# Kernel optimization log

Measured on AMD Instinct MI355X. Metric: run time of the kernel, lower is better.

Reference implementation:

```python
import jax, jax.numpy as jnp
import numpy as np

B, C, N = 32, 128, 64
HID = 2 * C
STEEPNESS = 50.0


def _bitonic_layers(n):
    """Index pairs (a, b) for each compare-exchange layer of a bitonic sorting
    network, matching diffsort's bitonic_network construction."""
    num_blocks = int(np.log2(n))
    assert n == 2 ** num_blocks
    layers = []
    for block in range(num_blocks):
        for layer in range(block + 1):
            m = 2 ** (block - layer)
            a_idx, b_idx = [], []
            for i in range(0, n, 2 * m):
                for j in range(m):
                    ix = i + j
                    a, b = ix, ix + m
                    # alternate direction within bitonic blocks
                    if (ix // 2 ** (block + 1)) % 2 == 1:
                        a, b = b, a
                    a_idx.append(a)
                    b_idx.append(b)
            layers.append((np.asarray(a_idx), np.asarray(b_idx)))
    return layers

_LAYERS = _bitonic_layers(N)  # 21 layers for N=64


def _diff_sort(scores):
    """Differentiable bitonic sort (diffsort, distribution='cauchy').
    Returns (soft-sorted scores, soft permutation matrix P) with
    sorted = scores @ P; the module applies P via bmm(P, rows)."""
    b, n = scores.shape
    x = scores
    P = jnp.broadcast_to(jnp.eye(n, dtype=scores.dtype), (b, n, n))
    inv_pi = 1.0 / np.pi
    for a_idx, b_idx in _LAYERS:
        xa, xb = x[:, a_idx], x[:, b_idx]
        alpha = jnp.arctan((xb - xa) * STEEPNESS) * inv_pi + 0.5  # Cauchy CDF
        x = x.at[:, a_idx].set(alpha * xa + (1.0 - alpha) * xb)
        x = x.at[:, b_idx].set((1.0 - alpha) * xa + alpha * xb)
        Pa, Pb = P[:, :, a_idx], P[:, :, b_idx]
        al = alpha[:, None, :]
        P = P.at[:, :, a_idx].set(al * Pa + (1.0 - al) * Pb)
        P = P.at[:, :, b_idx].set((1.0 - al) * Pa + al * Pb)
    return x, P


def setup_inputs() -> dict:
    key = jax.random.key(0)
    ks = jax.random.split(key, 9)
    s = 0.05  # keep score magnitudes reasonable under steepness=50
    return {
        "x": jax.random.normal(ks[0], (B, C, N, N), jnp.float32),
        "w1": jax.random.normal(ks[1], (HID, C), jnp.float32) * s,
        "b1": jax.random.normal(ks[2], (HID,), jnp.float32) * s,
        "w2": jax.random.normal(ks[3], (HID, HID), jnp.float32) * s,
        "b2": jax.random.normal(ks[4], (HID,), jnp.float32) * s,
        "w_row": jax.random.normal(ks[5], (HID, N), jnp.float32) * s,
        "b_row": jax.random.normal(ks[6], (1,), jnp.float32) * s,
        "w_col": jax.random.normal(ks[7], (HID, N), jnp.float32) * s,
        "b_col": jax.random.normal(ks[8], (1,), jnp.float32) * s,
    }


def reference(x, w1, b1, w2, b2, w_row, b_row, w_col, b_col):
    # feat_extractor: two 1x1 convs (pointwise channel GEMMs) + ReLU
    h = jax.nn.relu(jnp.einsum('bchw,oc->bohw', x, w1) + b1[None, :, None, None])
    h = jax.nn.relu(jnp.einsum('bchw,oc->bohw', h, w2) + b2[None, :, None, None])

    # row branch: Conv1d(HID*N,1,1) over flattened (channel, width) per row
    row_scores = jnp.einsum('bchw,cw->bh', h, w_row) + b_row  # (B, N)
    _, p_row = _diff_sort(row_scores)
    x = jnp.einsum('bij,bcjk->bcik', p_row, x)  # bmm(P_row, x) per channel

    # col branch: Conv1d(HID*N,1,1) over flattened (channel, height) per column
    col_scores = jnp.einsum('bchw,ch->bw', h, w_col) + b_col  # (B, N)
    _, p_col = _diff_sort(col_scores)
    # original: bmm(P_col, x^T) then view as (B,C,N,N) with NO transpose back
    x = jnp.einsum('bij,bckj->bcik', p_col, x)
    return x
```

## Files before the change

kernel.cpp:

```cpp
#include <hip/hip_runtime.h>
#include <math.h>

#define B_    32
#define C_    128
#define N_    64
#define HID_  256
#define PIX_  4096
#define STEEP 50.0f
#define INV_PI 0.318309886183790671f
#define LDH   272
#define LDX   72

typedef unsigned short u16;
typedef __attribute__((ext_vector_type(8))) short bf16x8;
typedef __attribute__((ext_vector_type(4))) float f32x4;

__device__ __forceinline__ u16 f2bf(float f) {
    unsigned int u = __builtin_bit_cast(unsigned int, f);
    unsigned int r = (u + 0x7FFFu + ((u >> 16) & 1u)) >> 16;
    return (u16)r;
}
__device__ __forceinline__ float bf2f(u16 h) {
    unsigned int u = ((unsigned int)h) << 16;
    return __builtin_bit_cast(float, u);
}
__device__ __forceinline__ int h1_idx(int p, int k) {
    return p * LDH + (((k >> 3) + (p & 7)) & 31) * 8 + (k & 7);
}
__device__ __forceinline__ int x_idx(int p, int k) {
    return p * LDH + 128 + (((k >> 3) + (p & 7)) & 15) * 8 + (k & 7);
}

__global__ void k_prep(const float* __restrict__ w1, const float* __restrict__ w2,
                       u16* __restrict__ w1h, u16* __restrict__ w1l,
                       u16* __restrict__ w2h, u16* __restrict__ w2l,
                       float* __restrict__ col_s, const float* __restrict__ b_col) {
    int i = blockIdx.x * 256 + threadIdx.x;
    if (i < B_ * N_) col_s[i] = b_col[0];
    if (i < HID_ * C_) {
        float v = w1[i];
        u16 h = f2bf(v);
        w1h[i] = h;
        w1l[i] = f2bf(v - bf2f(h));
    } else {
        int j = i - HID_ * C_;
        if (j < HID_ * HID_) {
            float v = w2[j];
            u16 h = f2bf(v);
            w2h[j] = h;
            w2l[j] = f2bf(v - bf2f(h));
        }
    }
}

__global__ __launch_bounds__(512) void k12_fused(
    const float* __restrict__ x,
    const u16* __restrict__ w1h, const u16* __restrict__ w1l,
    const float* __restrict__ b1,
    const u16* __restrict__ w2h, const u16* __restrict__ w2l,
    const float* __restrict__ b2, const float* __restrict__ w_row,
    const float* __restrict__ b_row, const float* __restrict__ w_col,
    float* __restrict__ row_s, float* __restrict__ col_s) {
    __shared__ __align__(16) u16 Lh[64 * LDH];
    __shared__ __align__(16) u16 Ll[64 * LDH];
    __shared__ float col_red[64];
    __shared__ float row_red;

    const int t = threadIdx.x;
    const int l = t & 63, w = t >> 6;
    const int col = l & 15, q = l >> 4;
    const int hrow = blockIdx.x;
    const int b = blockIdx.y;
    const float* xb = x + (size_t)b * C_ * PIX_ + hrow * 64;

    if (t < 64) col_red[t] = 0.f;
    if (t == 0) row_red = 0.f;

    {
        const int pt = t & 15, ct = t >> 4;
#pragma unroll
        for (int cc = 0; cc < 2; cc++) {
            const int c = cc * 64 + 2 * ct;
            float4 v0 = *(const float4*)&xb[(size_t)c * PIX_ + pt * 4];
            float4 v1 = *(const float4*)&xb[(size_t)(c + 1) * PIX_ + pt * 4];
            float a0[4] = {v0.x, v0.y, v0.z, v0.w};
            float a1[4] = {v1.x, v1.y, v1.z, v1.w};
#pragma unroll
            for (int j = 0; j < 4; j++) {
                int p = pt * 4 + j;
                u16 h0 = f2bf(a0[j]), h1v = f2bf(a1[j]);
                u16 l0 = f2bf(a0[j] - bf2f(h0)), l1 = f2bf(a1[j] - bf2f(h1v));
                int idx = x_idx(p, c);
                *(unsigned int*)&Lh[idx] = (unsigned int)h0 | ((unsigned int)h1v << 16);
                *(unsigned int*)&Ll[idx] = (unsigned int)l0 | ((unsigned int)l1 << 16);
            }
        }
    }
    __syncthreads();

    f32x4 acc[2][4];
#pragma unroll
    for (int i = 0; i < 2; i++)
#pragma unroll
        for (int j = 0; j < 4; j++) acc[i][j] = (f32x4){0.f, 0.f, 0.f, 0.f};

    bf16x8 ah[2], al_[2];
#pragma unroll
    for (int mf = 0; mf < 2; mf++) {
        size_t ro = (size_t)(32 * w + 16 * mf + col) * C_ + q * 8;
        ah[mf] = *(const bf16x8*)&w1h[ro];
        al_[mf] = *(const bf16x8*)&w1l[ro];
    }
#pragma unroll
    for (int kc = 0; kc < 4; kc++) {
        bf16x8 bh[4], bl[4];
#pragma unroll
        for (int nt = 0; nt < 4; nt++) {
            int idx = x_idx(nt * 16 + col, kc * 32 + q * 8);
            bh[nt] = *(const bf16x8*)&Lh[idx];
            bl[nt] = *(const bf16x8*)&Ll[idx];
        }
        bf16x8 ahn[2], aln[2];
        const int kn = (kc + 1) & 3;
#pragma unroll
        for (int mf = 0; mf < 2; mf++) {
            size_t ro = (size_t)(32 * w + 16 * mf + col) * C_ + kn * 32 + q * 8;
            ahn[mf] = *(const bf16x8*)&w1h[ro];
            aln[mf] = *(const bf16x8*)&w1l[ro];
        }
#pragma unroll
        for (int mf = 0; mf < 2; mf++)
#pragma unroll
            for (int nt = 0; nt < 4; nt++) {
                acc[mf][nt] = __builtin_amdgcn_mfma_f32_16x16x32_bf16(ah[mf], bh[nt], acc[mf][nt], 0, 0, 0);
                acc[mf][nt] = __builtin_amdgcn_mfma_f32_16x16x32_bf16(ah[mf], bl[nt], acc[mf][nt], 0, 0, 0);
                acc[mf][nt] = __builtin_amdgcn_mfma_f32_16x16x32_bf16(al_[mf], bh[nt], acc[mf][nt], 0, 0, 0);
            }
#pragma unroll
        for (int mf = 0; mf < 2; mf++) { ah[mf] = ahn[mf]; al_[mf] = aln[mf]; }
    }

    bf16x8 ah2[2], al2[2];
#pragma unroll
    for (int mf = 0; mf < 2; mf++) {
        size_t ro = (size_t)(32 * w + 16 * mf + col) * HID_ + q * 8;
        ah2[mf] = *(const bf16x8*)&w2h[ro];
        al2[mf] = *(const bf16x8*)&w2l[ro];
    }
    __syncthreads();

#pragma unroll
    for (int mf = 0; mf < 2; mf++) {
        int o = 32 * w + 16 * mf + q * 4;
        float bias[4];
#pragma unroll
        for (int r = 0; r < 4; r++) bias[r] = b1[o + r];
#pragma unroll
        for (int nt = 0; nt < 4; nt++) {
            int p = nt * 16 + col;
            u16 hh[4], ll[4];
#pragma unroll
            for (int r = 0; r < 4; r++) {
                float v = fmaxf(acc[mf][nt][r] + bias[r], 0.f);
                u16 h = f2bf(v);
                hh[r] = h;
                ll[r] = f2bf(v - bf2f(h));
            }
            int idx = h1_idx(p, o);
            *(unsigned long long*)&Lh[idx] =
                (unsigned long long)hh[0] | ((unsigned long long)hh[1] << 16) |
                ((unsigned long long)hh[2] << 32) | ((unsigned long long)hh[3] << 48);
            *(unsigned long long*)&Ll[idx] =
                (unsigned long long)ll[0] | ((unsigned long long)ll[1] << 16) |
                ((unsigned long long)ll[2] << 32) | ((unsigned long long)ll[3] << 48);
        }
    }
    __syncthreads();

    f32x4 acc2[2][4];
#pragma unroll
    for (int i = 0; i < 2; i++)
#pragma unroll
        for (int j = 0; j < 4; j++) acc2[i][j] = (f32x4){0.f, 0.f, 0.f, 0.f};

#pragma unroll
    for (int kc = 0; kc < 8; kc++) {
        bf16x8 bh[4], bl[4];
#pragma unroll
        for (int nt = 0; nt < 4; nt++) {
            int idx = h1_idx(nt * 16 + col, kc * 32 + q * 8);
            bh[nt] = *(const bf16x8*)&Lh[idx];
            bl[nt] = *(const bf16x8*)&Ll[idx];
        }
        bf16x8 ahn[2], aln[2];
        const int kn = (kc + 1) & 7;
#pragma unroll
        for (int mf = 0; mf < 2; mf++) {
            size_t ro = (size_t)(32 * w + 16 * mf + col) * HID_ + kn * 32 + q * 8;
            ahn[mf] = *(const bf16x8*)&w2h[ro];
            aln[mf] = *(const bf16x8*)&w2l[ro];
        }
#pragma unroll
        for (int mf = 0; mf < 2; mf++)
#pragma unroll
            for (int nt = 0; nt < 4; nt++) {
                acc2[mf][nt] = __builtin_amdgcn_mfma_f32_16x16x32_bf16(ah2[mf], bh[nt], acc2[mf][nt], 0, 0, 0);
                acc2[mf][nt] = __builtin_amdgcn_mfma_f32_16x16x32_bf16(ah2[mf], bl[nt], acc2[mf][nt], 0, 0, 0);
                acc2[mf][nt] = __builtin_amdgcn_mfma_f32_16x16x32_bf16(al2[mf], bh[nt], acc2[mf][nt], 0, 0, 0);
            }
#pragma unroll
        for (int mf = 0; mf < 2; mf++) { ah2[mf] = ahn[mf]; al2[mf] = aln[mf]; }
    }

    float rpart = 0.f;
    float cpart[4] = {0.f, 0.f, 0.f, 0.f};
#pragma unroll
    for (int mf = 0; mf < 2; mf++) {
        int o = 32 * w + 16 * mf + q * 4;
#pragma unroll
        for (int r = 0; r < 4; r++) {
            float bias = b2[o + r];
            float wcv = w_col[(o + r) * N_ + hrow];
#pragma unroll
            for (int nt = 0; nt < 4; nt++) {
                int wc = nt * 16 + col;
                float v = fmaxf(acc2[mf][nt][r] + bias, 0.f);
                rpart += v * w_row[(o + r) * N_ + wc];
                cpart[nt] += v * wcv;
            }
        }
    }
#pragma unroll
    for (int off = 32; off; off >>= 1) rpart += __shfl_xor(rpart, off, 64);
    if (l == 0) atomicAdd(&row_red, rpart);
#pragma unroll
    for (int nt = 0; nt < 4; nt++) {
        float cp = cpart[nt];
        cp += __shfl_xor(cp, 16, 64);
        cp += __shfl_xor(cp, 32, 64);
        if (l < 16) atomicAdd(&col_red[nt * 16 + l], cp);
    }
    __syncthreads();
    if (t < 64) atomicAdd(&col_s[b * N_ + t], col_red[t]);
    if (t == 0) row_s[b * N_ + hrow] = b_row[0] + row_red;
}

__global__ __launch_bounds__(256) void k4_diffsort(const float* __restrict__ row_s,
                                                   const float* __restrict__ col_s,
                                                   u16* __restrict__ prow_h, u16* __restrict__ prow_l,
                                                   u16* __restrict__ pcol_h, u16* __restrict__ pcol_l) {
    const int t = threadIdx.x;
    const int lane = t & 63, w = t >> 6;
    const int which = blockIdx.x & 1;
    const int b = blockIdx.x >> 1;
    const float* sc = which ? col_s : row_s;
    u16* Ph = which ? pcol_h : prow_h;
    u16* Pl = which ? pcol_l : prow_l;

    float xv = sc[b * 64 + lane];
    float P[16];
#pragma unroll
    for (int r = 0; r < 16; r++) P[r] = ((w * 16 + r) == lane) ? 1.f : 0.f;

#pragma unroll
    for (int bl = 0; bl < 6; bl++) {
#pragma unroll
        for (int ly = 0; ly <= bl; ly++) {
            const int sh = bl - ly;
            const int m = 1 << sh;
            float xp = __shfl_xor(xv, m, 64);
            int lower = ((lane >> sh) & 1) ^ 1;
            int swp = (lane >> (bl + 1)) & 1;
            float diff = (lower ^ swp) ? (xp - xv) : (xv - xp);
            float al = atanf(diff * STEEP) * INV_PI + 0.5f;
            xv = al * xv + (1.f - al) * xp;
#pragma unroll
            for (int r = 0; r < 16; r++) {
                float Pp = __shfl_xor(P[r], m, 64);
                P[r] = al * P[r] + (1.f - al) * Pp;
            }
        }
    }
#pragma unroll
    for (int r = 0; r < 16; r++) {
        float v = P[r];
        u16 h = f2bf(v);
        int row = w * 16 + r;
        Ph[(size_t)b * 4096 + row * 64 + lane] = h;
        Pl[(size_t)b * 4096 + row * 64 + lane] = f2bf(v - bf2f(h));
    }
}

__global__ __launch_bounds__(256) void k5_permute(const float* __restrict__ x,
                                                  const u16* __restrict__ pcol_h,
                                                  const u16* __restrict__ pcol_l,
                                                  const u16* __restrict__ prow_h,
                                                  const u16* __restrict__ prow_l,
                                                  float* __restrict__ out) {
    __shared__ __align__(16) u16 Xh[64 * LDX];
    __shared__ __align__(16) u16 Xl[64 * LDX];
    __shared__ __align__(16) u16 Zh[64 * LDX];
    __shared__ __align__(16) u16 Zl[64 * LDX];
    const int t = threadIdx.x;
    const int l = t & 63, w = t >> 6;
    const int col = l & 15, q = l >> 4;
    const int b = blockIdx.y;
    const int cbase = blockIdx.x * 4;
    const int i0 = w * 16;

    const u16* pch = pcol_h + (size_t)b * 4096;
    const u16* pcl = pcol_l + (size_t)b * 4096;
    const u16* prh = prow_h + (size_t)b * 4096;
    const u16* prl = prow_l + (size_t)b * 4096;

    bf16x8 pcA_h[2], pcA_l[2];
#pragma unroll
    for (int ks = 0; ks < 2; ks++) {
        pcA_h[ks] = *(const bf16x8*)&pch[(i0 + col) * 64 + q * 8 + ks * 32];
        pcA_l[ks] = *(const bf16x8*)&pcl[(i0 + col) * 64 + q * 8 + ks * 32];
    }
    bf16x8 prA_h[2][4], prA_l[2][4];
#pragma unroll
    for (int ks = 0; ks < 2; ks++)
#pragma unroll
        for (int ntj = 0; ntj < 4; ntj++) {
            prA_h[ks][ntj] = *(const bf16x8*)&prh[(ntj * 16 + col) * 64 + q * 8 + ks * 32];
            prA_l[ks][ntj] = *(const bf16x8*)&prl[(ntj * 16 + col) * 64 + q * 8 + ks * 32];
        }

    for (int ci = 0; ci < 4; ci++) {
        const int c = cbase + ci;
        const float* xc = x + ((size_t)b * C_ + c) * PIX_;
#pragma unroll
        for (int k = 0; k < 4; k++) {
            int f = t + k * 256;
            int rw = f >> 4, c4 = f & 15;
            float4 v = *(const float4*)&xc[f * 4];
            u16 h0 = f2bf(v.x), h1 = f2bf(v.y), h2 = f2bf(v.z), h3 = f2bf(v.w);
            ushort4 hv = {h0, h1, h2, h3};
            ushort4 lv = {f2bf(v.x - bf2f(h0)), f2bf(v.y - bf2f(h1)),
                          f2bf(v.z - bf2f(h2)), f2bf(v.w - bf2f(h3))};
            *(ushort4*)&Xh[rw * LDX + c4 * 4] = hv;
            *(ushort4*)&Xl[rw * LDX + c4 * 4] = lv;
        }
        __syncthreads();

        f32x4 acc[4];
#pragma unroll
        for (int nt = 0; nt < 4; nt++) acc[nt] = (f32x4){0.f, 0.f, 0.f, 0.f};
#pragma unroll
        for (int ks = 0; ks < 2; ks++) {
            bf16x8 ph = pcA_h[ks], pl = pcA_l[ks];
#pragma unroll
            for (int nt = 0; nt < 4; nt++) {
                bf16x8 xh8 = *(const bf16x8*)&Xh[(nt * 16 + col) * LDX + q * 8 + ks * 32];
                bf16x8 xl8 = *(const bf16x8*)&Xl[(nt * 16 + col) * LDX + q * 8 + ks * 32];
                acc[nt] = __builtin_amdgcn_mfma_f32_16x16x32_bf16(xh8, ph, acc[nt], 0, 0, 0);
                acc[nt] = __builtin_amdgcn_mfma_f32_16x16x32_bf16(xl8, ph, acc[nt], 0, 0, 0);
                acc[nt] = __builtin_amdgcn_mfma_f32_16x16x32_bf16(xh8, pl, acc[nt], 0, 0, 0);
            }
        }
#pragma unroll
        for (int nt = 0; nt < 4; nt++) {
            u16 hh[4], ll[4];
#pragma unroll
            for (int r = 0; r < 4; r++) {
                float v = acc[nt][r];
                u16 h = f2bf(v);
                hh[r] = h;
                ll[r] = f2bf(v - bf2f(h));
            }
            int zi = (i0 + col) * LDX + nt * 16 + q * 4;
            *(unsigned long long*)&Zh[zi] =
                (unsigned long long)hh[0] | ((unsigned long long)hh[1] << 16) |
                ((unsigned long long)hh[2] << 32) | ((unsigned long long)hh[3] << 48);
            *(unsigned long long*)&Zl[zi] =
                (unsigned long long)ll[0] | ((unsigned long long)ll[1] << 16) |
                ((unsigned long long)ll[2] << 32) | ((unsigned long long)ll[3] << 48);
        }

        f32x4 acc2[4];
#pragma unroll
        for (int nt = 0; nt < 4; nt++) acc2[nt] = (f32x4){0.f, 0.f, 0.f, 0.f};
#pragma unroll
        for (int ks = 0; ks < 2; ks++) {
            bf16x8 zh8 = *(const bf16x8*)&Zh[(i0 + col) * LDX + q * 8 + ks * 32];
            bf16x8 zl8 = *(const bf16x8*)&Zl[(i0 + col) * LDX + q * 8 + ks * 32];
#pragma unroll
            for (int ntj = 0; ntj < 4; ntj++) {
                acc2[ntj] = __builtin_amdgcn_mfma_f32_16x16x32_bf16(prA_h[ks][ntj], zh8, acc2[ntj], 0, 0, 0);
                acc2[ntj] = __builtin_amdgcn_mfma_f32_16x16x32_bf16(prA_l[ks][ntj], zh8, acc2[ntj], 0, 0, 0);
                acc2[ntj] = __builtin_amdgcn_mfma_f32_16x16x32_bf16(prA_h[ks][ntj], zl8, acc2[ntj], 0, 0, 0);
            }
        }
        float* oc = out + ((size_t)b * C_ + c) * PIX_;
#pragma unroll
        for (int ntj = 0; ntj < 4; ntj++) {
            float4 vv = {acc2[ntj][0], acc2[ntj][1], acc2[ntj][2], acc2[ntj][3]};
            *(float4*)&oc[(i0 + col) * 64 + ntj * 16 + q * 4] = vv;
        }
        __syncthreads();
    }
}

extern "C" void kernel_launch(void* const* d_in, const int* in_sizes, int n_in,
                              void* d_out, int out_size, void* d_ws, size_t ws_size,
                              hipStream_t stream) {
    const float* x = (const float*)d_in[0];
    const float* w1 = (const float*)d_in[1];
    const float* b1 = (const float*)d_in[2];
    const float* w2 = (const float*)d_in[3];
    const float* b2 = (const float*)d_in[4];
    const float* w_row = (const float*)d_in[5];
    const float* b_row = (const float*)d_in[6];
    const float* w_col = (const float*)d_in[7];
    const float* b_col = (const float*)d_in[8];
    float* out = (float*)d_out;

    char* ws = (char*)d_ws;
    u16* w1h = (u16*)(ws);
    u16* w1l = (u16*)(ws + 65536);
    u16* w2h = (u16*)(ws + 131072);
    u16* w2l = (u16*)(ws + 262144);
    float* row_s = (float*)(ws + 393216);
    float* col_s = (float*)(ws + 401408);
    u16* prow_h = (u16*)(ws + 409600);
    u16* prow_l = (u16*)(ws + 671744);
    u16* pcol_h = (u16*)(ws + 933888);
    u16* pcol_l = (u16*)(ws + 1196032);

    hipLaunchKernelGGL(k_prep, dim3(384), dim3(256), 0, stream, w1, w2, w1h, w1l, w2h, w2l,
                       col_s, b_col);
    hipLaunchKernelGGL(k12_fused, dim3(64, 32), dim3(512), 0, stream,
                       x, w1h, w1l, b1, w2h, w2l, b2, w_row, b_row, w_col, row_s, col_s);
    hipLaunchKernelGGL(k4_diffsort, dim3(64), dim3(256), 0, stream,
                       row_s, col_s, prow_h, prow_l, pcol_h, pcol_l);
    hipLaunchKernelGGL(k5_permute, dim3(32, 32), dim3(256), 0, stream,
                       x, pcol_h, pcol_l, prow_h, prow_l, out);
}
```

Measured before the change: 269.7 us.

## Double-buffer x tiles in permute kernel and keep intermediate in registers via 16x16x16 MFMA

The permute kernel now double-buffers the per-channel x tile in shared memory. It prefetches the next channel's data into registers while the current channel's MFMAs run, which removes one barrier per iteration. When the 16x16x16 bf16 MFMA builtin is available, the intermediate Z product is split to bf16 hi/lo directly from accumulator registers and fed as the B operand, skipping the shared-memory round trip. The x_idx swizzle for another kernel is also changed. The cost is more shared memory and register pressure, and the smaller-K MFMA issues more instructions.

```diff
diff --git a/kernel.cpp b/kernel.cpp
--- a/kernel.cpp
+++ b/kernel.cpp
@@ -11,8 +11,18 @@
 #define LDH   272
 #define LDX   72
 
+#if defined(__has_builtin)
+#if __has_builtin(__builtin_amdgcn_mfma_f32_16x16x16bf16_1k)
+#define HAVE_MFMA16 1
+#endif
+#endif
+#ifndef HAVE_MFMA16
+#define HAVE_MFMA16 0
+#endif
+
 typedef unsigned short u16;
 typedef __attribute__((ext_vector_type(8))) short bf16x8;
+typedef __attribute__((ext_vector_type(4))) short bf16x4;
 typedef __attribute__((ext_vector_type(4))) float f32x4;
 
 __device__ __forceinline__ u16 f2bf(float f) {
@@ -28,7 +38,7 @@
     return p * LDH + (((k >> 3) + (p & 7)) & 31) * 8 + (k & 7);
 }
 __device__ __forceinline__ int x_idx(int p, int k) {
-    return p * LDH + 128 + (((k >> 3) + (p & 7)) & 15) * 8 + (k & 7);
+    return p * LDH + 128 + (((k >> 3) + ((p >> 2) & 7)) & 15) * 8 + (k & 7);
 }
 
 __global__ void k_prep(const float* __restrict__ w1, const float* __restrict__ w2,
@@ -297,10 +307,12 @@
                                                   const u16* __restrict__ prow_h,
                                                   const u16* __restrict__ prow_l,
                                                   float* __restrict__ out) {
-    __shared__ __align__(16) u16 Xh[64 * LDX];
-    __shared__ __align__(16) u16 Xl[64 * LDX];
+    __shared__ __align__(16) u16 Xh[2][64 * LDX];
+    __shared__ __align__(16) u16 Xl[2][64 * LDX];
+#if !HAVE_MFMA16
     __shared__ __align__(16) u16 Zh[64 * LDX];
     __shared__ __align__(16) u16 Zl[64 * LDX];
+#endif
     const int t = threadIdx.x;
     const int l = t & 63, w = t >> 6;
     const int col = l & 15, q = l >> 4;
@@ -319,6 +331,16 @@
         pcA_h[ks] = *(const bf16x8*)&pch[(i0 + col) * 64 + q * 8 + ks * 32];
         pcA_l[ks] = *(const bf16x8*)&pcl[(i0 + col) * 64 + q * 8 + ks * 32];
     }
+#if HAVE_MFMA16
+    bf16x4 prH[4][4], prL[4][4];
+#pragma unroll
+    for (int kc = 0; kc < 4; kc++)
+#pragma unroll
+        for (int ntj = 0; ntj < 4; ntj++) {
+            prH[kc][ntj] = *(const bf16x4*)&prh[(ntj * 16 + col) * 64 + kc * 16 + q * 4];
+            prL[kc][ntj] = *(const bf16x4*)&prl[(ntj * 16 + col) * 64 + kc * 16 + q * 4];
+        }
+#else
     bf16x8 prA_h[2][4], prA_l[2][4];
 #pragma unroll
     for (int ks = 0; ks < 2; ks++)
@@ -327,10 +349,10 @@
             prA_h[ks][ntj] = *(const bf16x8*)&prh[(ntj * 16 + col) * 64 + q * 8 + ks * 32];
             prA_l[ks][ntj] = *(const bf16x8*)&prl[(ntj * 16 + col) * 64 + q * 8 + ks * 32];
         }
-
-    for (int ci = 0; ci < 4; ci++) {
-        const int c = cbase + ci;
-        const float* xc = x + ((size_t)b * C_ + c) * PIX_;
+#endif
+
+    {
+        const float* xc = x + ((size_t)b * C_ + cbase) * PIX_;
 #pragma unroll
         for (int k = 0; k < 4; k++) {
             int f = t + k * 256;
@@ -340,10 +362,21 @@
             ushort4 hv = {h0, h1, h2, h3};
             ushort4 lv = {f2bf(v.x - bf2f(h0)), f2bf(v.y - bf2f(h1)),
                           f2bf(v.z - bf2f(h2)), f2bf(v.w - bf2f(h3))};
-            *(ushort4*)&Xh[rw * LDX + c4 * 4] = hv;
-            *(ushort4*)&Xl[rw * LDX + c4 * 4] = lv;
-        }
+            *(ushort4*)&Xh[0][rw * LDX + c4 * 4] = hv;
+            *(ushort4*)&Xl[0][rw * LDX + c4 * 4] = lv;
+        }
+    }
+
+    for (int ci = 0; ci < 4; ci++) {
+        const int cur = ci & 1;
         __syncthreads();
+
+        float4 pv[4];
+        if (ci < 3) {
+            const float* xcn = x + ((size_t)b * C_ + cbase + ci + 1) * PIX_;
+#pragma unroll
+            for (int k = 0; k < 4; k++) pv[k] = *(const float4*)&xcn[(t + k * 256) * 4];
+        }
 
         f32x4 acc[4];
 #pragma unroll
@@ -353,13 +386,38 @@
             bf16x8 ph = pcA_h[ks], pl = pcA_l[ks];
 #pragma unroll
             for (int nt = 0; nt < 4; nt++) {
-                bf16x8 xh8 = *(const bf16x8*)&Xh[(nt * 16 + col) * LDX + q * 8 + ks * 32];
-                bf16x8 xl8 = *(const bf16x8*)&Xl[(nt * 16 + col) * LDX + q * 8 + ks * 32];
+                bf16x8 xh8 = *(const bf16x8*)&Xh[cur][(nt * 16 + col) * LDX + q * 8 + ks * 32];
+                bf16x8 xl8 = *(const bf16x8*)&Xl[cur][(nt * 16 + col) * LDX + q * 8 + ks * 32];
                 acc[nt] = __builtin_amdgcn_mfma_f32_16x16x32_bf16(xh8, ph, acc[nt], 0, 0, 0);
                 acc[nt] = __builtin_amdgcn_mfma_f32_16x16x32_bf16(xl8, ph, acc[nt], 0, 0, 0);
                 acc[nt] = __builtin_amdgcn_mfma_f32_16x16x32_bf16(xh8, pl, acc[nt], 0, 0, 0);
             }
         }
+
+        f32x4 acc2[4];
+#pragma unroll
+        for (int nt = 0; nt < 4; nt++) acc2[nt] = (f32x4){0.f, 0.f, 0.f, 0.f};
+#if HAVE_MFMA16
+        bf16x4 zH[4], zL[4];
+#pragma unroll
+        for (int kc = 0; kc < 4; kc++) {
+#pragma unroll
+            for (int j = 0; j < 4; j++) {
+                float v = acc[kc][j];
+                u16 h = f2bf(v);
+                zH[kc][j] = (short)h;
+                zL[kc][j] = (short)f2bf(v - bf2f(h));
+            }
+        }
+#pragma unroll
+        for (int kc = 0; kc < 4; kc++)
+#pragma unroll
+            for (int ntj = 0; ntj < 4; ntj++) {
+                acc2[ntj] = __builtin_amdgcn_mfma_f32_16x16x16bf16_1k(prH[kc][ntj], zH[kc], acc2[ntj], 0, 0, 0);
+                acc2[ntj] = __builtin_amdgcn_mfma_f32_16x16x16bf16_1k(prL[kc][ntj], zH[kc], acc2[ntj], 0, 0, 0);
+                acc2[ntj] = __builtin_amdgcn_mfma_f32_16x16x16bf16_1k(prH[kc][ntj], zL[kc], acc2[ntj], 0, 0, 0);
+            }
+#else
 #pragma unroll
         for (int nt = 0; nt < 4; nt++) {
             u16 hh[4], ll[4];
@@ -378,10 +436,6 @@
                 (unsigned long long)ll[0] | ((unsigned long long)ll[1] << 16) |
                 ((unsigned long long)ll[2] << 32) | ((unsigned long long)ll[3] << 48);
         }
-
-        f32x4 acc2[4];
-#pragma unroll
-        for (int nt = 0; nt < 4; nt++) acc2[nt] = (f32x4){0.f, 0.f, 0.f, 0.f};
 #pragma unroll
         for (int ks = 0; ks < 2; ks++) {
             bf16x8 zh8 = *(const bf16x8*)&Zh[(i0 + col) * LDX + q * 8 + ks * 32];
@@ -393,13 +447,29 @@
                 acc2[ntj] = __builtin_amdgcn_mfma_f32_16x16x32_bf16(prA_h[ks][ntj], zl8, acc2[ntj], 0, 0, 0);
             }
         }
-        float* oc = out + ((size_t)b * C_ + c) * PIX_;
+#endif
+        float* oc = out + ((size_t)b * C_ + cbase + ci) * PIX_;
 #pragma unroll
         for (int ntj = 0; ntj < 4; ntj++) {
             float4 vv = {acc2[ntj][0], acc2[ntj][1], acc2[ntj][2], acc2[ntj][3]};
             *(float4*)&oc[(i0 + col) * 64 + ntj * 16 + q * 4] = vv;
         }
-        __syncthreads();
+
+        if (ci < 3) {
+            const int nxt = cur ^ 1;
+#pragma unroll
+            for (int k = 0; k < 4; k++) {
+                int f = t + k * 256;
+                int rw = f >> 4, c4 = f & 15;
+                float4 v = pv[k];
+                u16 h0 = f2bf(v.x), h1 = f2bf(v.y), h2 = f2bf(v.z), h3 = f2bf(v.w);
+                ushort4 hv = {h0, h1, h2, h3};
+                ushort4 lv = {f2bf(v.x - bf2f(h0)), f2bf(v.y - bf2f(h1)),
+                              f2bf(v.z - bf2f(h2)), f2bf(v.w - bf2f(h3))};
+                *(ushort4*)&Xh[nxt][rw * LDX + c4 * 4] = hv;
+                *(ushort4*)&Xl[nxt][rw * LDX + c4 * 4] = lv;
+            }
+        }
     }
 }
 
```

After: 257.1 us. 1.05x faster.
